# Kernel optimization log

Hardware: AMD Instinct MI355X
Metric: run time of the kernel (lower is better)

The kernel has to match this reference:

```python
import jax, jax.numpy as jnp
import numpy as np

B, T, E, H = 64, 512, 512, 64
NEG_INF = jnp.float32(-1e30)


def setup_inputs() -> dict:
    key = jax.random.key(0)
    kx, kk, kq, kv = jax.random.split(key, 4)
    x = jax.random.normal(kx, (B, T, E), dtype=jnp.float32)
    attn_mask = jnp.ones((B, T), dtype=jnp.int32)
    Wk = jax.random.normal(kk, (E, H), dtype=jnp.float32) * (E ** -0.5)
    Wq = jax.random.normal(kq, (E, H), dtype=jnp.float32) * (E ** -0.5)
    Wv = jax.random.normal(kv, (E, H), dtype=jnp.float32) * (E ** -0.5)
    return {"x": x, "attn_mask": attn_mask, "Wk": Wk, "Wq": Wq, "Wv": Wv}


def reference(x, attn_mask, Wk, Wq, Wv):
    # x: (B,T,E); projections to (B,T,H)
    k = x @ Wk
    q = x @ Wq
    v = x @ Wv
    # scaled attention scores (B,T,T)
    wei = jnp.einsum('bth,bsh->bts', q, k) * (H ** -0.5)
    t = x.shape[1]
    causal = jnp.tril(jnp.ones((t, t), dtype=bool))  # (T,T)
    wei = jnp.where(causal[None, :, :], wei, NEG_INF)
    # padding mask: attn_mask (B,T) broadcast over query dim (matches unsqueeze(1).expand)
    wei = jnp.where(attn_mask[:, None, :] != 0, wei, NEG_INF)
    wei = jax.nn.softmax(wei, axis=-1)
    # dropout omitted (eval mode) for deterministic correctness baseline
    return jnp.einsum('bts,bsh->bth', wei, v)
```

## Files before the change

### kernel.cpp

```cpp
#include <hip/hip_runtime.h>

#define B 64
#define T 512
#define E 512
#define H 64
#define NEG_INF (-1e30f)

#define PBM 64
#define PN 192

#define QSCALE 0.18033688011112043f
#define DEFER_THR 8.0f

using short8 = __attribute__((ext_vector_type(8))) short;
using f32x16 = __attribute__((ext_vector_type(16))) float;

__device__ __forceinline__ unsigned short f2bf(float f) {
    unsigned int u = __float_as_uint(f);
    u += 0x7fffu + ((u >> 16) & 1u);
    return (unsigned short)(u >> 16);
}
__device__ __forceinline__ unsigned int bfpack_tr(float lo, float hi) {
    return (__float_as_uint(hi) & 0xffff0000u) | (__float_as_uint(lo) >> 16);
}

__global__ __launch_bounds__(256) void prep(
    const float* __restrict__ Wq, const float* __restrict__ Wk,
    const float* __restrict__ Wv, const int* __restrict__ am,
    unsigned short* __restrict__ wfrag, unsigned int* __restrict__ mbits)
{
    const int bid = blockIdx.x;
    if (bid < 384) {
        const int i  = bid * 256 + threadIdx.x;
        const int f  = i >> 9;
        const int le = i & 511;
        const int ln = le >> 3, e = le & 7;
        const int ko = ln >> 5, rr = ln & 31;
        const int c  = f / 24;
        const int ks = (f - c * 24) / 6;
        const int ct = f % 6;
        const int col = ct * 32 + rr;
        const int kk  = c * 64 + ks * 16 + ko * 8 + e;
        const int seg = col >> 6, hh = col & 63;
        const float* W = (seg == 0) ? Wq : (seg == 1) ? Wk : Wv;
        float v = W[(size_t)kk * H + hh];
        if (seg == 0) v *= QSCALE;
        wfrag[i] = f2bf(v);
    } else {
        const int i = (bid - 384) * 256 + threadIdx.x;
        const unsigned long long bal = __ballot(am[i] != 0);
        const int lane = threadIdx.x & 63;
        if (lane == 0)       mbits[i >> 5] = (unsigned int)bal;
        else if (lane == 32) mbits[i >> 5] = (unsigned int)(bal >> 32);
    }
}

__global__ __launch_bounds__(384, 3) void proj_gemm(
    const float* __restrict__ x,
    const unsigned short* __restrict__ wfrag,
    unsigned short* __restrict__ qfrag, unsigned short* __restrict__ kfrag,
    unsigned short* __restrict__ vfrag)
{
    __shared__ unsigned short Xs[PBM * 512];

    const int tid  = threadIdx.x;
    const int w    = tid >> 6;
    const int lane = tid & 63;
    const int hi   = lane >> 5;
    const int r    = lane & 31;
    const int row0 = blockIdx.x * PBM;

    {
        float4 A[13], Bq[13];
        #pragma unroll
        for (int d = 0; d < 2; ++d) {
            const int i = d * 384 + tid;
            if (i < 4096) {
                const float4* s = reinterpret_cast<const float4*>(
                    &x[(size_t)(row0 + (i >> 6)) * E + (i & 63) * 8]);
                A[d] = s[0]; Bq[d] = s[1];
            }
        }
        #pragma unroll
        for (int st = 0; st < 11; ++st) {
            if (st + 2 < 11) {
                const int i = (st + 2) * 384 + tid;
                if (i < 4096) {
                    const float4* s = reinterpret_cast<const float4*>(
                        &x[(size_t)(row0 + (i >> 6)) * E + (i & 63) * 8]);
                    A[st + 2] = s[0]; Bq[st + 2] = s[1];
                }
            }
            const int i = st * 384 + tid;
            if (i < 4096) {
                const int rr = i >> 6, g = i & 63;
                union { unsigned short us[8]; short8 v; } pk;
                pk.us[0] = f2bf(A[st].x);  pk.us[1] = f2bf(A[st].y);
                pk.us[2] = f2bf(A[st].z);  pk.us[3] = f2bf(A[st].w);
                pk.us[4] = f2bf(Bq[st].x); pk.us[5] = f2bf(Bq[st].y);
                pk.us[6] = f2bf(Bq[st].z); pk.us[7] = f2bf(Bq[st].w);
                *reinterpret_cast<short8*>(
                    (char*)Xs + rr * 1024 + ((g + rr) & 63) * 16) = pk.v;
            }
        }
    }

    short8 breg[16];
    #pragma unroll
    for (int c = 0; c < 4; ++c)
        #pragma unroll
        for (int ks = 0; ks < 4; ++ks)
            breg[c * 4 + ks] = *reinterpret_cast<const short8*>(
                wfrag + ((size_t)((c * 4 + ks) * 6 + w)) * 512 + lane * 8);

    __syncthreads();

    f32x16 acc[2] = {};

    #pragma unroll
    for (int c = 0; c < 4; ++c) {
        #pragma unroll
        for (int mt = 0; mt < 2; ++mt) {
            const int mrow = mt * 32 + r;
            #pragma unroll
            for (int ks = 0; ks < 4; ++ks) {
                const int g = c * 8 + ks * 2 + hi;
                const short8 a = *reinterpret_cast<const short8*>(
                    (const char*)Xs + mrow * 1024 + ((g + mrow) & 63) * 16);
                acc[mt] = __builtin_amdgcn_mfma_f32_32x32x16_bf16(
                    a, breg[c * 4 + ks], acc[mt], 0, 0, 0);
            }
        }
    }

    #pragma unroll
    for (int c = 0; c < 4; ++c)
        #pragma unroll
        for (int ks = 0; ks < 4; ++ks)
            breg[c * 4 + ks] = *reinterpret_cast<const short8*>(
                wfrag + ((size_t)(((c + 4) * 4 + ks) * 6 + w)) * 512 + lane * 8);

    #pragma unroll
    for (int c = 0; c < 4; ++c) {
        #pragma unroll
        for (int mt = 0; mt < 2; ++mt) {
            const int mrow = mt * 32 + r;
            #pragma unroll
            for (int ks = 0; ks < 4; ++ks) {
                const int g = (c + 4) * 8 + ks * 2 + hi;
                const short8 a = *reinterpret_cast<const short8*>(
                    (const char*)Xs + mrow * 1024 + ((g + mrow) & 63) * 16);
                acc[mt] = __builtin_amdgcn_mfma_f32_32x32x16_bf16(
                    a, breg[c * 4 + ks], acc[mt], 0, 0, 0);
            }
        }
    }

    const int gc  = w * 32 + r;
    const int seg = gc >> 6;
    const int h   = gc & 63;
    #pragma unroll
    for (int mt = 0; mt < 2; ++mt) {
        #pragma unroll
        for (int reg = 0; reg < 16; ++reg) {
            const int drow = (reg & 3) + 8 * (reg >> 2) + 4 * hi;
            const int grow = row0 + mt * 32 + drow;
            const float val = acc[mt][reg];
            const int bb  = grow >> 9;
            const int key = grow & 511;
            const int blk = key >> 5;
            const int kk  = key & 31;
            if (seg == 0) {
                qfrag[(((size_t)bb * 16 + blk) * 4 + (h >> 4)) * 512
                      + (((h >> 3) & 1) * 32 + kk) * 8 + (h & 7)] = f2bf(val);
            } else if (seg == 1) {
                kfrag[(((size_t)bb * 16 + blk) * 4 + (h >> 4)) * 512
                      + (((h >> 3) & 1) * 32 + kk) * 8 + (h & 7)] = f2bf(val);
            } else {
                vfrag[(((size_t)bb * 16 + blk) * 4 + ((kk >> 4) * 2 + (h >> 5))) * 512
                      + (((kk >> 3) & 1) * 32 + (h & 31)) * 8 + (kk & 7)] = f2bf(val);
            }
        }
    }
}

__global__ __launch_bounds__(256) void attn_online(
    const unsigned short* __restrict__ qfrag,
    const unsigned short* __restrict__ kfrag,
    const unsigned short* __restrict__ vfrag,
    const unsigned int* __restrict__ mbits,
    float* __restrict__ out)
{
    __shared__ float mlS[4][2][32];
    __shared__ float Ob[4][32][68];

    const int tid  = threadIdx.x;
    const int w    = tid >> 6;
    const int lane = tid & 63;
    const int hi = lane >> 5, r = lane & 31;
    const int h4 = 4 * hi;

    const int bid = blockIdx.x;
    const int kk2 = bid >> 3;
    const int b   = ((kk2 >> 4) << 3) | (bid & 7);
    const int s   = 15 - (kk2 & 15);
    const int t0  = s * 32;
    const int tq  = t0 + r;
    const int l8  = lane * 8;

    f32x16 accO[2] = {};
    float m = -INFINITY, l = 0.f;

    if (w <= s) {
        short8 qf[4];
        {
            const unsigned short* qb = qfrag + (((size_t)b * 16 + s) * 4) * 512;
            #pragma unroll
            for (int ks = 0; ks < 4; ++ks)
                qf[ks] = *reinterpret_cast<const short8*>(qb + ks * 512 + l8);
        }
        short8 kf[4], vb[4];
        {
            const unsigned short* kb = kfrag + (((size_t)b * 16 + w) * 4) * 512;
            const unsigned short* vv = vfrag + (((size_t)b * 16 + w) * 4) * 512;
            #pragma unroll
            for (int ks = 0; ks < 4; ++ks) {
                kf[ks] = *reinterpret_cast<const short8*>(kb + ks * 512 + l8);
                vb[ks] = *reinterpret_cast<const short8*>(vv + ks * 512 + l8);
            }
        }

        for (int j = w; j <= s; j += 4) {
            short8 kn[4], vn[4];
            if (j + 4 <= s) {
                const unsigned short* kb = kfrag + (((size_t)b * 16 + j + 4) * 4) * 512;
                const unsigned short* vv = vfrag + (((size_t)b * 16 + j + 4) * 4) * 512;
                #pragma unroll
                for (int ks = 0; ks < 4; ++ks) {
                    kn[ks] = *reinterpret_cast<const short8*>(kb + ks * 512 + l8);
                    vn[ks] = *reinterpret_cast<const short8*>(vv + ks * 512 + l8);
                }
            }

            __builtin_amdgcn_s_setprio(1);
            f32x16 sc = {};
            #pragma unroll
            for (int ks = 0; ks < 4; ++ks)
                sc = __builtin_amdgcn_mfma_f32_32x32x16_bf16(kf[ks], qf[ks], sc, 0, 0, 0);
            __builtin_amdgcn_s_setprio(0);

            const unsigned int mw = mbits[b * 16 + j];
            const bool fullm = (mw == 0xffffffffu);
            float cmax = -INFINITY;
            if (j == s) {
                #pragma unroll
                for (int reg = 0; reg < 16; ++reg) {
                    const int cr = (reg & 3) + 8 * (reg >> 2) + h4;
                    float v = sc[reg];
                    const bool bad = (32 * j + cr > tq) || (!fullm && !((mw >> cr) & 1u));
                    v = bad ? NEG_INF : v;
                    sc[reg] = v;
                    cmax = fmaxf(cmax, v);
                }
            } else if (fullm) {
                #pragma unroll
                for (int reg = 0; reg < 16; ++reg)
                    cmax = fmaxf(cmax, sc[reg]);
            } else {
                #pragma unroll
                for (int reg = 0; reg < 16; ++reg) {
                    const int cr = (reg & 3) + 8 * (reg >> 2) + h4;
                    float v = sc[reg];
                    v = ((mw >> cr) & 1u) ? v : NEG_INF;
                    sc[reg] = v;
                    cmax = fmaxf(cmax, v);
                }
            }
            cmax = fmaxf(cmax, __shfl_xor(cmax, 32));

            if (!__all(cmax <= m + DEFER_THR)) {
                const float m_new = fmaxf(m, cmax);
                const float scale = exp2f(m - m_new);
                f32x16 scf;
                #pragma unroll
                for (int reg = 0; reg < 16; ++reg)
                    scf[reg] = __shfl(scale, (reg & 3) + 8 * (reg >> 2) + h4);
                #pragma unroll
                for (int reg = 0; reg < 16; ++reg) {
                    accO[0][reg] *= scf[reg];
                    accO[1][reg] *= scf[reg];
                }
                l *= scale;
                m = m_new;
            }

            float csum = 0.f;
            #pragma unroll
            for (int reg = 0; reg < 16; ++reg) {
                const float p = exp2f(sc[reg] - m);
                sc[reg] = p;
                csum += p;
            }
            csum += __shfl_xor(csum, 32);
            l += csum;

            unsigned int pk[8];
            #pragma unroll
            for (int jj = 0; jj < 8; ++jj)
                pk[jj] = bfpack_tr(sc[2 * jj], sc[2 * jj + 1]);
            __builtin_amdgcn_s_setprio(1);
            #pragma unroll
            for (int hs = 0; hs < 2; ++hs) {
                const unsigned int p01 = pk[hs * 4 + 0], p23 = pk[hs * 4 + 1];
                const unsigned int p45 = pk[hs * 4 + 2], p67 = pk[hs * 4 + 3];
                const unsigned int sendA = hi ? p01 : p45;
                const unsigned int sendB = hi ? p23 : p67;
                const unsigned int recvA = (unsigned int)__shfl_xor((int)sendA, 32);
                const unsigned int recvB = (unsigned int)__shfl_xor((int)sendB, 32);
                union { unsigned int uu[4]; short8 s8; } aw;
                aw.uu[0] = hi ? recvA : p01;
                aw.uu[1] = hi ? recvB : p23;
                aw.uu[2] = hi ? p45 : recvA;
                aw.uu[3] = hi ? p67 : recvB;
                #pragma unroll
                for (int tile = 0; tile < 2; ++tile)
                    accO[tile] = __builtin_amdgcn_mfma_f32_32x32x16_bf16(
                        aw.s8, vb[hs * 2 + tile], accO[tile], 0, 0, 0);
            }
            __builtin_amdgcn_s_setprio(0);

            #pragma unroll
            for (int ks = 0; ks < 4; ++ks) { kf[ks] = kn[ks]; vb[ks] = vn[ks]; }
        }
    }

    if (hi == 0) { mlS[w][0][r] = m; mlS[w][1][r] = l; }
    #pragma unroll
    for (int reg = 0; reg < 16; ++reg) {
        const int qrow = (reg & 3) + 8 * (reg >> 2) + h4;
        Ob[w][qrow][r]      = accO[0][reg];
        Ob[w][qrow][r + 32] = accO[1][reg];
    }
    __syncthreads();

    {
        const int row = tid >> 3;
        const int c8  = (tid & 7) * 8;

        float mi[4], li[4];
        float mstar = -INFINITY;
        #pragma unroll
        for (int w2 = 0; w2 < 4; ++w2) {
            mi[w2] = mlS[w2][0][row];
            li[w2] = mlS[w2][1][row];
            mstar = fmaxf(mstar, mi[w2]);
        }
        float L = 0.f, fw[4];
        #pragma unroll
        for (int w2 = 0; w2 < 4; ++w2) {
            fw[w2] = exp2f(mi[w2] - mstar);
            L += fw[w2] * li[w2];
        }
        const float inv = 1.f / L;

        float acc[8] = {};
        #pragma unroll
        for (int w2 = 0; w2 < 4; ++w2) {
            const float4 lo = *reinterpret_cast<const float4*>(&Ob[w2][row][c8]);
            const float4 hi4v = *reinterpret_cast<const float4*>(&Ob[w2][row][c8 + 4]);
            acc[0] += fw[w2] * lo.x;  acc[1] += fw[w2] * lo.y;
            acc[2] += fw[w2] * lo.z;  acc[3] += fw[w2] * lo.w;
            acc[4] += fw[w2] * hi4v.x; acc[5] += fw[w2] * hi4v.y;
            acc[6] += fw[w2] * hi4v.z; acc[7] += fw[w2] * hi4v.w;
        }

        float* op = &out[((size_t)b * T + t0 + row) * H + c8];
        float4 o0 = { acc[0] * inv, acc[1] * inv, acc[2] * inv, acc[3] * inv };
        float4 o1 = { acc[4] * inv, acc[5] * inv, acc[6] * inv, acc[7] * inv };
        *reinterpret_cast<float4*>(op)     = o0;
        *reinterpret_cast<float4*>(op + 4) = o1;
    }
}

extern "C" void kernel_launch(void* const* d_in, const int* in_sizes, int n_in,
                              void* d_out, int out_size, void* d_ws, size_t ws_size,
                              hipStream_t stream) {
    const float* x         = (const float*)d_in[0];
    const int*   attn_mask = (const int*)d_in[1];
    const float* Wk        = (const float*)d_in[2];
    const float* Wq        = (const float*)d_in[3];
    const float* Wv        = (const float*)d_in[4];
    float* out = (float*)d_out;

    unsigned short* qfrag = (unsigned short*)d_ws;
    unsigned short* kfrag = qfrag + (size_t)B * T * H;
    unsigned short* vfrag = kfrag + (size_t)B * T * H;
    unsigned short* wfrag = vfrag + (size_t)B * T * H;
    unsigned int*   mbits = (unsigned int*)(wfrag + (size_t)PN * E);

    prep<<<512, 256, 0, stream>>>(Wq, Wk, Wv, attn_mask, wfrag, mbits);
    proj_gemm<<<(B * T) / PBM, 384, 0, stream>>>(x, wfrag, qfrag, kfrag, vfrag);
    attn_online<<<B * 16, 256, 0, stream>>>(qfrag, kfrag, vfrag, mbits, out);
}
```

Measured before the change: 49.30 us.

## Pipeline x staging through double-buffered K-chunks in projection GEMM

The projection GEMM used to stage a full 64x512 bf16 tile of x into shared memory before computing. It now streams 64-wide K chunks through a small double-buffered LDS tile, prefetching two chunks ahead into registers so global loads and bf16 conversion overlap with MFMA work. This cuts LDS use from 64KB to 16KB and drops the min-blocks launch bound. The cost is a barrier per chunk, only 256 of 384 threads doing the staging, and possibly higher register pressure.

```diff
diff --git a/kernel.cpp b/kernel.cpp
--- a/kernel.cpp
+++ b/kernel.cpp
@@ -7,7 +7,9 @@
 #define NEG_INF (-1e30f)
 
 #define PBM 64
+#define PBK 64
 #define PN 192
+#define NCHK (E / PBK)
 
 #define QSCALE 0.18033688011112043f
 #define DEFER_THR 8.0f
@@ -23,6 +25,10 @@
 __device__ __forceinline__ unsigned int bfpack_tr(float lo, float hi) {
     return (__float_as_uint(hi) & 0xffff0000u) | (__float_as_uint(lo) >> 16);
 }
+
+#define LGKM_BARRIER() do { asm volatile("s_waitcnt lgkmcnt(0)" ::: "memory"); \
+                            __builtin_amdgcn_s_barrier(); \
+                            __builtin_amdgcn_sched_barrier(0); } while (0)
 
 __global__ __launch_bounds__(256) void prep(
     const float* __restrict__ Wq, const float* __restrict__ Wk,
@@ -55,13 +61,13 @@
     }
 }
 
-__global__ __launch_bounds__(384, 3) void proj_gemm(
+__global__ __launch_bounds__(384) void proj_gemm(
     const float* __restrict__ x,
     const unsigned short* __restrict__ wfrag,
     unsigned short* __restrict__ qfrag, unsigned short* __restrict__ kfrag,
     unsigned short* __restrict__ vfrag)
 {
-    __shared__ unsigned short Xs[PBM * 512];
+    __shared__ unsigned short Xs[2][PBM * 64];
 
     const int tid  = threadIdx.x;
     const int w    = tid >> 6;
@@ -69,41 +75,14 @@
     const int hi   = lane >> 5;
     const int r    = lane & 31;
     const int row0 = blockIdx.x * PBM;
-
-    {
-        float4 A[13], Bq[13];
-        #pragma unroll
-        for (int d = 0; d < 2; ++d) {
-            const int i = d * 384 + tid;
-            if (i < 4096) {
-                const float4* s = reinterpret_cast<const float4*>(
-                    &x[(size_t)(row0 + (i >> 6)) * E + (i & 63) * 8]);
-                A[d] = s[0]; Bq[d] = s[1];
-            }
-        }
-        #pragma unroll
-        for (int st = 0; st < 11; ++st) {
-            if (st + 2 < 11) {
-                const int i = (st + 2) * 384 + tid;
-                if (i < 4096) {
-                    const float4* s = reinterpret_cast<const float4*>(
-                        &x[(size_t)(row0 + (i >> 6)) * E + (i & 63) * 8]);
-                    A[st + 2] = s[0]; Bq[st + 2] = s[1];
-                }
-            }
-            const int i = st * 384 + tid;
-            if (i < 4096) {
-                const int rr = i >> 6, g = i & 63;
-                union { unsigned short us[8]; short8 v; } pk;
-                pk.us[0] = f2bf(A[st].x);  pk.us[1] = f2bf(A[st].y);
-                pk.us[2] = f2bf(A[st].z);  pk.us[3] = f2bf(A[st].w);
-                pk.us[4] = f2bf(Bq[st].x); pk.us[5] = f2bf(Bq[st].y);
-                pk.us[6] = f2bf(Bq[st].z); pk.us[7] = f2bf(Bq[st].w);
-                *reinterpret_cast<short8*>(
-                    (char*)Xs + rr * 1024 + ((g + rr) & 63) * 16) = pk.v;
-            }
-        }
-    }
+    const bool stager = (tid < 256);
+
+    const int aXorBase[2] = { ((0 * 32 + r) & 7) << 4, ((1 * 32 + r) & 7) << 4 };
+    const int aBase2[2]   = { (0 * 32 + r) * 128, (1 * 32 + r) * 128 };
+
+    const int xs_rr0 = tid >> 3;
+    const int xs_rr1 = (256 + tid) >> 3;
+    const int xs_s16 = tid & 7;
 
     short8 breg[16];
     #pragma unroll
@@ -113,46 +92,89 @@
             breg[c * 4 + ks] = *reinterpret_cast<const short8*>(
                 wfrag + ((size_t)((c * 4 + ks) * 6 + w)) * 512 + lane * 8);
 
-    __syncthreads();
-
     f32x16 acc[2] = {};
+    float4 xA[2][2], xB[2][2];
+
+    if (stager) {
+        #pragma unroll
+        for (int p = 0; p < 2; ++p) {
+            const int rr = p ? xs_rr1 : xs_rr0;
+            const float4* src = reinterpret_cast<const float4*>(
+                &x[(size_t)(row0 + rr) * E + xs_s16 * 8]);
+            const float4 a0 = src[0], a1 = src[1];
+            union { unsigned short us[8]; short8 v; } pk;
+            pk.us[0] = f2bf(a0.x); pk.us[1] = f2bf(a0.y);
+            pk.us[2] = f2bf(a0.z); pk.us[3] = f2bf(a0.w);
+            pk.us[4] = f2bf(a1.x); pk.us[5] = f2bf(a1.y);
+            pk.us[6] = f2bf(a1.z); pk.us[7] = f2bf(a1.w);
+            const int cb = (xs_s16 * 16) ^ ((rr & 7) << 4);
+            *reinterpret_cast<short8*>((char*)(&Xs[0][0]) + rr * 128 + cb) = pk.v;
+        }
+        #pragma unroll
+        for (int p = 0; p < 2; ++p) {
+            const int rr = p ? xs_rr1 : xs_rr0;
+            const float4* src = reinterpret_cast<const float4*>(
+                &x[(size_t)(row0 + rr) * E + PBK + xs_s16 * 8]);
+            xA[1][p] = src[0];
+            xB[1][p] = src[1];
+        }
+    }
+    LGKM_BARRIER();
 
     #pragma unroll
-    for (int c = 0; c < 4; ++c) {
+    for (int c = 0; c < NCHK; ++c) {
+        const int cur = c & 1;
+
+        if (stager && c + 2 < NCHK) {
+            const int kc = (c + 2) * PBK;
+            #pragma unroll
+            for (int p = 0; p < 2; ++p) {
+                const int rr = p ? xs_rr1 : xs_rr0;
+                const float4* src = reinterpret_cast<const float4*>(
+                    &x[(size_t)(row0 + rr) * E + kc + xs_s16 * 8]);
+                xA[cur][p] = src[0];
+                xB[cur][p] = src[1];
+            }
+        }
+
         #pragma unroll
         for (int mt = 0; mt < 2; ++mt) {
-            const int mrow = mt * 32 + r;
             #pragma unroll
             for (int ks = 0; ks < 4; ++ks) {
-                const int g = c * 8 + ks * 2 + hi;
+                const int koff = ks * 32 + hi * 16;
                 const short8 a = *reinterpret_cast<const short8*>(
-                    (const char*)Xs + mrow * 1024 + ((g + mrow) & 63) * 16);
+                    (const char*)(&Xs[cur][0]) + aBase2[mt] + (koff ^ aXorBase[mt]));
                 acc[mt] = __builtin_amdgcn_mfma_f32_32x32x16_bf16(
-                    a, breg[c * 4 + ks], acc[mt], 0, 0, 0);
-            }
-        }
-    }
-
-    #pragma unroll
-    for (int c = 0; c < 4; ++c)
-        #pragma unroll
-        for (int ks = 0; ks < 4; ++ks)
-            breg[c * 4 + ks] = *reinterpret_cast<const short8*>(
-                wfrag + ((size_t)(((c + 4) * 4 + ks) * 6 + w)) * 512 + lane * 8);
-
-    #pragma unroll
-    for (int c = 0; c < 4; ++c) {
-        #pragma unroll
-        for (int mt = 0; mt < 2; ++mt) {
-            const int mrow = mt * 32 + r;
-            #pragma unroll
-            for (int ks = 0; ks < 4; ++ks) {
-                const int g = (c + 4) * 8 + ks * 2 + hi;
-                const short8 a = *reinterpret_cast<const short8*>(
-                    (const char*)Xs + mrow * 1024 + ((g + mrow) & 63) * 16);
-                acc[mt] = __builtin_amdgcn_mfma_f32_32x32x16_bf16(
-                    a, breg[c * 4 + ks], acc[mt], 0, 0, 0);
-            }
+                    a, breg[(c & 3) * 4 + ks], acc[mt], 0, 0, 0);
+            }
+        }
+
+        if (c == 3) {
+            #pragma unroll
+            for (int cc = 0; cc < 4; ++cc)
+                #pragma unroll
+                for (int ks = 0; ks < 4; ++ks)
+                    breg[cc * 4 + ks] = *reinterpret_cast<const short8*>(
+                        wfrag + ((size_t)(((cc + 4) * 4 + ks) * 6 + w)) * 512 + lane * 8);
+        }
+
+        if (c + 1 < NCHK) {
+            if (stager) {
+                const int nb = (c + 1) & 1;
+                #pragma unroll
+                for (int p = 0; p < 2; ++p) {
+                    const int rr = p ? xs_rr1 : xs_rr0;
+                    union { unsigned short us[8]; short8 v; } pk;
+                    pk.us[0] = f2bf(xA[nb][p].x); pk.us[1] = f2bf(xA[nb][p].y);
+                    pk.us[2] = f2bf(xA[nb][p].z); pk.us[3] = f2bf(xA[nb][p].w);
+                    pk.us[4] = f2bf(xB[nb][p].x); pk.us[5] = f2bf(xB[nb][p].y);
+                    pk.us[6] = f2bf(xB[nb][p].z); pk.us[7] = f2bf(xB[nb][p].w);
+                    const int cb = (xs_s16 * 16) ^ ((rr & 7) << 4);
+                    *reinterpret_cast<short8*>(
+                        (char*)(&Xs[cur ^ 1][0]) + rr * 128 + cb) = pk.v;
+                }
+            }
+            LGKM_BARRIER();
         }
     }
 
```

After: 48.41 us. Within noise of the previous version (-1.8%).
